# Kernel tuning notes

Measured on AMD Instinct MI355X. Metric: run time of the kernel, lower is better.

The kernel has to match this reference:

```python
import jax, jax.numpy as jnp
import numpy as np

EPS = 1e-12  # matches torch F.normalize default eps


def _l2_normalize(x):
    # torch F.normalize(x, dim=2): x / max(||x||_2, eps)
    n = jnp.sqrt(jnp.sum(x * x, axis=2, keepdims=True))
    return x / jnp.maximum(n, EPS)


def setup_inputs() -> dict:
    key = jax.random.key(0)
    k1, k2 = jax.random.split(key)
    B, C, HW = 8, 1024, 3136
    fm_s = jax.random.normal(k1, (B, C, HW), dtype=jnp.float32)
    fm_t = jax.random.normal(k2, (B, C, HW), dtype=jnp.float32)
    return {"fm_s": fm_s, "fm_t": fm_t}


def reference(fm_s, fm_t):
    s = _l2_normalize(fm_s)  # (B, C, HW)
    t = _l2_normalize(fm_t)  # (B, C, HW)
    # poly_kernel(a, b) = (a[:,None,:,:] * b[:,:,None,:]).sum(-1)**2
    # == (b @ a^T)**2 computed as a batched matmul -> (B, C, C)
    k_ss = jnp.einsum('bnc,bmc->bnm', s, s) ** 2
    k_st = jnp.einsum('bnc,bmc->bnm', t, s) ** 2
    return jnp.mean(k_ss) - 2.0 * jnp.mean(k_st)
```

## Files before the change

### kernel.cpp

```cpp
#include <hip/hip_runtime.h>
#include <stdint.h>

typedef __attribute__((ext_vector_type(4)))  int   i32x4;
typedef __attribute__((ext_vector_type(8)))  int   i32x8;
typedef __attribute__((ext_vector_type(16))) float f32x16;

#define NB 8
#define NC 1024
#define NHW 3136
#define ROWB8 3200

__device__ inline float sq4(float4 v){
  return fmaf(v.x,v.x, fmaf(v.y,v.y, fmaf(v.z,v.z, v.w*v.w)));
}

__device__ __forceinline__ void load_lds16(const void* g, void* l){
  __builtin_amdgcn_global_load_lds(
      (const __attribute__((address_space(1))) unsigned int*)g,
      (__attribute__((address_space(3))) unsigned int*)l,
      16, 0, 0);
}

__device__ __forceinline__ f32x16 MFS(i32x8 a, i32x8 b, f32x16 c){
  return __builtin_amdgcn_mfma_scale_f32_32x32x64_f8f6f4(
      a, b, c, 0, 0, 0, 0x7F7F7F7F, 0, 0x7F7F7F7F);
}

__device__ __forceinline__ i32x8 rdfrag(const char* base, int cLo, int cHi){
  i32x4 lo = *(const i32x4*)(base + cLo);
  i32x4 hi = *(const i32x4*)(base + cHi);
  return __builtin_shufflevector(lo, hi, 0,1,2,3,4,5,6,7);
}

__device__ __forceinline__ int cvt4(float4 v, float s){
  int pk = __builtin_amdgcn_cvt_pk_fp8_f32(v.x*s, v.y*s, 0,  0);
  pk     = __builtin_amdgcn_cvt_pk_fp8_f32(v.z*s, v.w*s, pk, 1);
  return pk;
}

__global__ __launch_bounds__(256, 8) void k_norm(const float* __restrict__ s,
                                                 const float* __restrict__ t,
                                                 char* __restrict__ Sn,
                                                 char* __restrict__ Tn,
                                                 float* __restrict__ accbuf){
  __shared__ float4 buf[784];
  __shared__ float red[4];
  const int g   = blockIdx.x;
  const int tid = threadIdx.x;
  if (g == 0 && tid == 0){ accbuf[0] = 0.f; accbuf[1] = 0.f; }
  const bool isS = (g < 8192);
  const int r = isS ? g : g - 8192;
  const float* src = (isS ? s : t) + (size_t)r * NHW;
  char*        dst = (isS ? Sn : Tn) + (size_t)r * ROWB8;

  {
    const char* gp = (const char*)src + tid*16;
    char*       lp = (char*)buf + tid*16;
    load_lds16(gp,         lp);
    load_lds16(gp +  4096, lp +  4096);
    load_lds16(gp +  8192, lp +  8192);
    if (tid < 16) load_lds16(gp + 12288, lp + 12288);
  }
  asm volatile("s_waitcnt vmcnt(0)" ::: "memory");
  __syncthreads();

  float ssq = sq4(buf[tid]) + sq4(buf[tid+256]) + sq4(buf[tid+512]);
  if (tid < 16) ssq += sq4(buf[tid+768]);
  #pragma unroll
  for (int off = 32; off; off >>= 1) ssq += __shfl_down(ssq, off);
  if ((tid & 63) == 0) red[tid>>6] = ssq;
  __syncthreads();
  const float inv = 32.0f / fmaxf(sqrtf(red[0]+red[1]+red[2]+red[3]), 1e-12f);

  *(int*)(dst + 4*tid)        = cvt4(buf[tid],     inv);
  *(int*)(dst + 4*tid + 1024) = cvt4(buf[tid+256], inv);
  *(int*)(dst + 4*tid + 2048) = cvt4(buf[tid+512], inv);
  if (tid < 16)      *(int*)(dst + 3072 + 4*tid) = cvt4(buf[tid+768], inv);
  else if (tid < 20) *(int4*)(dst + 3136 + 16*(tid-16)) = make_int4(0,0,0,0);
}


#define BAR   __builtin_amdgcn_s_barrier()
#define LGKM0 asm volatile("s_waitcnt lgkmcnt(0)" ::: "memory")
#define LGKM8 asm volatile("s_waitcnt lgkmcnt(8)" ::: "memory")
#define VM6   asm volatile("s_waitcnt vmcnt(6)" ::: "memory")
#define SB0   __builtin_amdgcn_sched_barrier(0)
#define PRIO1 __builtin_amdgcn_s_setprio(1)
#define PRIO0 __builtin_amdgcn_s_setprio(0)

#define ISSUE(MAT, D, H, KT) do{ \
  const char* _g = ((MAT)? gB : gA) + (KT)*128 + (H)*(128*ROWB8); \
  char* _d = ldsw + (D)*65536 + (MAT)*32768 + (H)*16384; \
  load_lds16(_g,              _d); \
  load_lds16(_g + 64*ROWB8,   _d + 8192); \
}while(0)

#define RDA(D, MH) do{ \
  const char* _a = aRow + (D) + (MH)*8192; \
  af[0][0] = rdfrag(_a,        c00, c01); \
  af[0][1] = rdfrag(_a,        c10, c11); \
  af[1][0] = rdfrag(_a + 4096, c00, c01); \
  af[1][1] = rdfrag(_a + 4096, c10, c11); \
}while(0)

#define RDB(D, NH) do{ \
  const char* _b = bRow + (D) + (NH)*4096; \
  bf[NH][0] = rdfrag(_b, c00, c01); \
  bf[NH][1] = rdfrag(_b, c10, c11); \
}while(0)

#define MMQ(MH, NH) do{ \
  acc[((MH)*2+0)*2+(NH)] = MFS(af[0][0], bf[NH][0], acc[((MH)*2+0)*2+(NH)]); \
  acc[((MH)*2+1)*2+(NH)] = MFS(af[1][0], bf[NH][0], acc[((MH)*2+1)*2+(NH)]); \
  acc[((MH)*2+0)*2+(NH)] = MFS(af[0][1], bf[NH][1], acc[((MH)*2+0)*2+(NH)]); \
  acc[((MH)*2+1)*2+(NH)] = MFS(af[1][1], bf[NH][1], acc[((MH)*2+1)*2+(NH)]); \
}while(0)

__global__ __launch_bounds__(512,2) void k_gemm(const char* __restrict__ Sn,
                                                const char* __restrict__ Tn,
                                                float* __restrict__ accbuf){
  __shared__ char lds[131072];
  const int tid = threadIdx.x;
  const int l   = tid & 63;
  const int w   = tid >> 6;
  const int wr  = w >> 2;
  const int wc  = w & 3;

  const int b   = blockIdx.x & 7;
  const int idx = blockIdx.x >> 3;
  int tm, tn, which; float wgt;
  if (idx < 16){ which = 1; tm = idx >> 2; tn = idx & 3; wgt = 1.f; }
  else {
    int e = idx - 16; which = 0;
    if      (e < 4){ tm = 0; tn = e;   }
    else if (e < 7){ tm = 1; tn = e-3; }
    else if (e < 9){ tm = 2; tn = e-5; }
    else           { tm = 3; tn = 3;   }
    wgt = (tm == tn) ? 1.f : 2.f;
  }
  const char* Ab = (which ? Tn : Sn) + (size_t)b*(NC*ROWB8) + (size_t)tm*(256*ROWB8);
  const char* Bb = Sn                + (size_t)b*(NC*ROWB8) + (size_t)tn*(256*ROWB8);

  const int scol = ((l & 7) << 4) ^ ((l >> 3) << 4);
  const char* gA = Ab + (8*w + (l >> 3))*ROWB8 + scol;
  const char* gB = Bb + (8*w + (l >> 3))*ROWB8 + scol;
  char* ldsw = lds + w*1024;

  const int swz = (l & 7) << 4;
  const int cg  = 32*(l >> 5);
  const int c00 = ( cg           ) ^ swz;
  const int c01 = ( cg | 16      ) ^ swz;
  const int c10 = ( cg | 64      ) ^ swz;
  const int c11 = ( cg | 64 | 16 ) ^ swz;
  const char* aRow = lds +         (wr*128 + (l & 31))*128;
  const char* bRow = lds + 32768 + (wc*64  + (l & 31))*128;

  i32x8 af[2][2], bf[2][2];
  f32x16 acc[8];
  #pragma unroll
  for (int i = 0; i < 8; i++) acc[i] = (f32x16){};

  ISSUE(1,0,0,0); ISSUE(1,0,1,0); ISSUE(0,0,0,0); ISSUE(0,0,1,0);
  ISSUE(1,1,0,1); ISSUE(1,1,1,1); ISSUE(0,1,0,1);
  VM6; BAR;

  for (int i = 0; i < 12; i++){
    const int t1 = 2*i + 1;
    const int t2 = 2*i + 2;
    int t3 = 2*i + 3; if (t3 > 24) t3 = 24;

    RDA(0,0); RDB(0,0);
    ISSUE(0,1,1,t1);
    LGKM8; BAR; LGKM0; SB0; PRIO1; MMQ(0,0); PRIO0; BAR;
    RDB(0,1);
    BAR; LGKM0; SB0; PRIO1; MMQ(0,1); PRIO0; BAR;
    RDA(0,1);
    ISSUE(1,0,0,t2); ISSUE(1,0,1,t2);
    BAR; LGKM0; SB0; PRIO1; MMQ(1,0); PRIO0; BAR;
    ISSUE(0,0,0,t2);
    BAR; PRIO1; MMQ(1,1); PRIO0; VM6; BAR;

    RDA(65536,0); RDB(65536,0);
    ISSUE(0,0,1,t2);
    LGKM8; BAR; LGKM0; SB0; PRIO1; MMQ(0,0); PRIO0; BAR;
    RDB(65536,1);
    BAR; LGKM0; SB0; PRIO1; MMQ(0,1); PRIO0; BAR;
    RDA(65536,1);
    ISSUE(1,1,0,t3); ISSUE(1,1,1,t3);
    BAR; LGKM0; SB0; PRIO1; MMQ(1,0); PRIO0; BAR;
    ISSUE(0,1,0,t3);
    BAR; PRIO1; MMQ(1,1); PRIO0; VM6; BAR;
  }

  RDA(0,0); RDB(0,0); RDB(0,1);
  MMQ(0,0); MMQ(0,1);
  RDA(0,1);
  MMQ(1,0); MMQ(1,1);

  float p = 0.f;
  #pragma unroll
  for (int f = 0; f < 8; f++)
    #pragma unroll
    for (int e = 0; e < 16; e++)
      p = fmaf(acc[f][e], acc[f][e], p);
  #pragma unroll
  for (int off = 32; off; off >>= 1) p += __shfl_down(p, off);
  __syncthreads();
  float* red = (float*)lds;
  if (l == 0) red[w] = p;
  __syncthreads();
  if (tid == 0){
    float sum = red[0]+red[1]+red[2]+red[3]+red[4]+red[5]+red[6]+red[7];
    atomicAdd(&accbuf[which], wgt * sum);
  }
}

__global__ void k_fin(const float* __restrict__ acc, float* __restrict__ out){
  out[0] = (acc[0] - 2.0f*acc[1]) * 1.1368683772161603e-13f;
}

extern "C" void kernel_launch(void* const* d_in, const int* in_sizes, int n_in,
                              void* d_out, int out_size, void* d_ws, size_t ws_size,
                              hipStream_t stream){
  const float* fs = (const float*)d_in[0];
  const float* ft = (const float*)d_in[1];
  float* out = (float*)d_out;
  float* accbuf = (float*)d_ws;
  char* Sn = (char*)d_ws + 256;
  char* Tn = Sn + (size_t)NB*NC*ROWB8;

  k_norm<<<dim3(16384), dim3(256), 0, stream>>>(fs, ft, Sn, Tn, accbuf);
  k_gemm<<<dim3(208), dim3(512), 0, stream>>>(Sn, Tn, accbuf);
  k_fin<<<1, 1, 0, stream>>>(accbuf, out);
}
```

Baseline: 85.47 us.

## Make normalization kernel persistent with double-buffered LDS prefetch of next row

```diff
diff --git a/kernel.cpp b/kernel.cpp
--- a/kernel.cpp
+++ b/kernel.cpp
@@ -9,6 +9,8 @@
 #define NC 1024
 #define NHW 3136
 #define ROWB8 3200
+#define NROWS 16384
+#define NGRID 1280
 
 __device__ inline float sq4(float4 v){
   return fmaf(v.x,v.x, fmaf(v.y,v.y, fmaf(v.z,v.z, v.w*v.w)));
@@ -38,55 +40,71 @@
   return pk;
 }
 
-__global__ __launch_bounds__(256, 8) void k_norm(const float* __restrict__ s,
-                                                 const float* __restrict__ t,
-                                                 char* __restrict__ Sn,
-                                                 char* __restrict__ Tn,
-                                                 float* __restrict__ accbuf){
-  __shared__ float4 buf[784];
-  __shared__ float red[4];
-  const int g   = blockIdx.x;
-  const int tid = threadIdx.x;
-  if (g == 0 && tid == 0){ accbuf[0] = 0.f; accbuf[1] = 0.f; }
-  const bool isS = (g < 8192);
-  const int r = isS ? g : g - 8192;
-  const float* src = (isS ? s : t) + (size_t)r * NHW;
-  char*        dst = (isS ? Sn : Tn) + (size_t)r * ROWB8;
-
-  {
-    const char* gp = (const char*)src + tid*16;
-    char*       lp = (char*)buf + tid*16;
-    load_lds16(gp,         lp);
-    load_lds16(gp +  4096, lp +  4096);
-    load_lds16(gp +  8192, lp +  8192);
-    if (tid < 16) load_lds16(gp + 12288, lp + 12288);
-  }
-  asm volatile("s_waitcnt vmcnt(0)" ::: "memory");
-  __syncthreads();
-
-  float ssq = sq4(buf[tid]) + sq4(buf[tid+256]) + sq4(buf[tid+512]);
-  if (tid < 16) ssq += sq4(buf[tid+768]);
-  #pragma unroll
-  for (int off = 32; off; off >>= 1) ssq += __shfl_down(ssq, off);
-  if ((tid & 63) == 0) red[tid>>6] = ssq;
-  __syncthreads();
-  const float inv = 32.0f / fmaxf(sqrtf(red[0]+red[1]+red[2]+red[3]), 1e-12f);
-
-  *(int*)(dst + 4*tid)        = cvt4(buf[tid],     inv);
-  *(int*)(dst + 4*tid + 1024) = cvt4(buf[tid+256], inv);
-  *(int*)(dst + 4*tid + 2048) = cvt4(buf[tid+512], inv);
-  if (tid < 16)      *(int*)(dst + 3072 + 4*tid) = cvt4(buf[tid+768], inv);
-  else if (tid < 20) *(int4*)(dst + 3136 + 16*(tid-16)) = make_int4(0,0,0,0);
-}
-
-
 #define BAR   __builtin_amdgcn_s_barrier()
 #define LGKM0 asm volatile("s_waitcnt lgkmcnt(0)" ::: "memory")
 #define LGKM8 asm volatile("s_waitcnt lgkmcnt(8)" ::: "memory")
 #define VM6   asm volatile("s_waitcnt vmcnt(6)" ::: "memory")
+#define VM4   asm volatile("s_waitcnt vmcnt(4)" ::: "memory")
+#define VM0   asm volatile("s_waitcnt vmcnt(0)" ::: "memory")
 #define SB0   __builtin_amdgcn_sched_barrier(0)
 #define PRIO1 __builtin_amdgcn_s_setprio(1)
 #define PRIO0 __builtin_amdgcn_s_setprio(0)
+
+__global__ __launch_bounds__(256) void k_norm(const float* __restrict__ s,
+                                              const float* __restrict__ t,
+                                              char* __restrict__ Sn,
+                                              char* __restrict__ Tn,
+                                              float* __restrict__ accbuf){
+  __shared__ char nbuf[2][13312];
+  __shared__ float red[4];
+  const int tid = threadIdx.x;
+  const int l   = tid & 63;
+  const int w   = tid >> 6;
+  if (blockIdx.x == 0 && tid == 0){ accbuf[0] = 0.f; accbuf[1] = 0.f; }
+
+#define NSRC(r) ((const char*)(((r) < 8192 ? s : t) + (size_t)((r) < 8192 ? (r) : (r)-8192) * NHW))
+#define NDST(r) (((r) < 8192 ? Sn : Tn) + (size_t)((r) < 8192 ? (r) : (r)-8192) * ROWB8)
+#define NISSUE(gsrc, lbase) do{ \
+    const char* _g = (gsrc); char* _l = (lbase); \
+    load_lds16(_g + tid*16,         _l + tid*16); \
+    load_lds16(_g + tid*16 +  4096, _l + tid*16 +  4096); \
+    load_lds16(_g + tid*16 +  8192, _l + tid*16 +  8192); \
+    load_lds16(_g + ((l < 16) ? 12288 + l*16 : l*16), _l + 12288 + l*16); \
+  }while(0)
+
+  int row = blockIdx.x;
+  if (row >= NROWS) return;
+  NISSUE(NSRC(row), nbuf[0]);
+  int cur = 0;
+  for (; row < NROWS; row += NGRID, cur ^= 1){
+    int nrow = row + NGRID; if (nrow >= NROWS) nrow = row;
+    BAR;
+    NISSUE(NSRC(nrow), nbuf[cur ^ 1]);
+    VM4;
+    BAR; SB0;
+
+    const float4* B = (const float4*)nbuf[cur];
+    float ssq = sq4(B[tid]) + sq4(B[tid+256]) + sq4(B[tid+512]);
+    if (tid < 16) ssq += sq4(B[768 + tid]);
+    #pragma unroll
+    for (int off = 32; off; off >>= 1) ssq += __shfl_down(ssq, off);
+    if ((tid & 63) == 0) red[w] = ssq;
+    LGKM0; BAR;
+    const float inv = 32.0f / fmaxf(sqrtf(red[0]+red[1]+red[2]+red[3]), 1e-12f);
+
+    char* dst = NDST(row);
+    *(int*)(dst + 4*tid)        = cvt4(B[tid],     inv);
+    *(int*)(dst + 4*tid + 1024) = cvt4(B[tid+256], inv);
+    *(int*)(dst + 4*tid + 2048) = cvt4(B[tid+512], inv);
+    if (tid < 16)      *(int*)(dst + 3072 + 4*tid) = cvt4(B[768+tid], inv);
+    else if (tid < 20) *(int4*)(dst + 3136 + 16*(tid-16)) = make_int4(0,0,0,0);
+  }
+  VM0;
+#undef NISSUE
+#undef NSRC
+#undef NDST
+}
+
 
 #define ISSUE(MAT, D, H, KT) do{ \
   const char* _g = ((MAT)? gB : gA) + (KT)*128 + (H)*(128*ROWB8); \
@@ -229,7 +247,7 @@
   char* Sn = (char*)d_ws + 256;
   char* Tn = Sn + (size_t)NB*NC*ROWB8;
 
-  k_norm<<<dim3(16384), dim3(256), 0, stream>>>(fs, ft, Sn, Tn, accbuf);
+  k_norm<<<dim3(NGRID), dim3(256), 0, stream>>>(fs, ft, Sn, Tn, accbuf);
   k_gemm<<<dim3(208), dim3(512), 0, stream>>>(Sn, Tn, accbuf);
   k_fin<<<1, 1, 0, stream>>>(accbuf, out);
 }
```

Result: slower. 87.96 us (+2.9%).
